# Performance work log

Measured on AMD Instinct MI355X. Metric: run time of the kernel, lower is better.

Reference implementation:

```python
import jax, jax.numpy as jnp
import numpy as np

B, T, C = 2, 2048, 1024
N_HEAD = 16
G_NON = 32   # qgroup_size_non (layernorm / residual path)
G_LIN = 32   # qgroup_size_lin (linear path)
QMAX = 127.0
EPS = 1e-5


def quantize(x, G):
    """Group-wise symmetric int8 quantization along the last dim.
    Returns q (int8, same shape as x) and scales s with shape x.shape[:-1] + (D//G,)."""
    shp = x.shape
    xg = x.reshape(shp[:-1] + (shp[-1] // G, G))
    s = jnp.maximum(jnp.max(jnp.abs(xg), axis=-1) / QMAX, 1e-8)
    q = jnp.clip(jnp.round(xg / s[..., None]), -QMAX, QMAX).astype(jnp.int8)
    return q.reshape(shp), s


def dequant(q, s, G):
    shp = q.shape
    xg = q.astype(jnp.float32).reshape(shp[:-1] + (shp[-1] // G, G)) * s[..., None]
    return xg.reshape(shp)


def quant_dequant(x, G):
    """Fake-quantize (straight-through): forward = dequant(quantize(x))."""
    q, s = quantize(x, G)
    xd = dequant(q, s, G)
    return x + jax.lax.stop_gradient(xd - x)


def setup_inputs() -> dict:
    key = jax.random.key(0)
    k1, k2, k3, k4 = jax.random.split(key, 4)
    x = jax.random.normal(k1, (B, T, C), dtype=jnp.float32)
    # LN stats of x, produced by the previous block's int8_add_..._MeanVar
    mean = jnp.mean(x, axis=-1)
    rstd = 1.0 / jnp.sqrt(jnp.var(x, axis=-1) + EPS)
    qx, sx = quantize(x, G_NON)
    ln_w = 1.0 + 0.02 * jax.random.normal(k2, (C,), dtype=jnp.float32)
    w1 = 0.02 * jax.random.normal(k3, (3 * C, C), dtype=jnp.float32)   # c_attn.weight [out,in]
    w2 = 0.02 * jax.random.normal(k4, (C, C), dtype=jnp.float32)       # c_proj.weight [out,in]
    return {"x": x, "qx": qx.astype(jnp.int32), "sx": sx, "mean": mean,
            "rstd": rstd, "ln_w": ln_w, "w1": w1, "w2": w2}


def reference(x, qx, sx, mean, rstd, ln_w, w1, w2):
    hd = C // N_HEAD
    # ---- Part1: int8 layernorm (uses provided mean/rstd) + int8 c_attn linear ----
    ln_in = dequant(qx.astype(jnp.int8), sx, G_NON)               # [B,T,C]
    h = (ln_in - mean[..., None]) * rstd[..., None] * ln_w        # layernorm output
    hq = quant_dequant(h, G_NON)                                  # requantize activations
    w1q = quant_dequant(w1, G_LIN)                                # int8 weight
    qkv = jnp.einsum('btc,oc->bto', hq, w1q)                      # [B,T,3C]
    q, k, v = jnp.split(qkv, 3, axis=-1)
    q = q.reshape(B, T, N_HEAD, hd).transpose(0, 2, 1, 3)         # [B,H,T,hd]
    k = k.reshape(B, T, N_HEAD, hd).transpose(0, 2, 1, 3)
    v = v.reshape(B, T, N_HEAD, hd).transpose(0, 2, 1, 3)
    # ---- causal SDPA ----
    scores = jnp.einsum('bhqd,bhkd->bhqk', q, k) / jnp.sqrt(jnp.float32(hd))
    causal = jnp.tril(jnp.ones((T, T), dtype=bool))
    scores = jnp.where(causal, scores, jnp.float32(-1e30))
    attn = jax.nn.softmax(scores, axis=-1)
    y = jnp.einsum('bhqk,bhkd->bhqd', attn, v)
    y = y.transpose(0, 2, 1, 3).reshape(B, T, C)
    # ---- Part2: int8 c_proj linear + residual add with mean/var ----
    yq = quant_dequant(y, G_LIN)
    w2q = quant_dequant(w2, G_LIN)
    proj = jnp.einsum('btc,oc->bto', yq, w2q)
    fpx = x + proj                                                # fp residual output
    mean_o = jnp.mean(fpx, axis=-1)
    rstd_o = 1.0 / jnp.sqrt(jnp.var(fpx, axis=-1) + EPS)
    qo, so = quantize(fpx, G_NON)                                 # quantized output for next block
    return (fpx, qo, so, mean_o, rstd_o)
```

## Files before the change

kernel.cpp:

```cpp
#include <hip/hip_runtime.h>
#include <stdint.h>

#define BB 2
#define TT 2048
#define CC 1024
#define NH 16
#define HD 64
#define NG 32
#define ROWS (BB*TT)
#define C3 (3*CC)

typedef _Float16 half_t;
typedef __attribute__((ext_vector_type(8))) _Float16 half8;
typedef __attribute__((ext_vector_type(2))) __fp16 fp16x2;
typedef __attribute__((ext_vector_type(4))) float f32x4;

#define GLDS16(g, l) __builtin_amdgcn_global_load_lds( \
    (__attribute__((address_space(1))) void*)(g), \
    (__attribute__((address_space(3))) void*)(l), 16, 0, 0)

#define LOG2E 1.44269504f
#define DEFER_THR 5.5451774f

__device__ __forceinline__ uint32_t pk_h2(float a, float b) {
  union { fp16x2 h; uint32_t u; } cv;
  cv.h = __builtin_amdgcn_cvt_pkrtz(a, b);
  return cv.u;
}

__global__ void k_qdq_w(const float* __restrict__ w1, const float* __restrict__ w2,
                        half_t* __restrict__ o1, half_t* __restrict__ o2) {
  int g = blockIdx.x * blockDim.x + threadIdx.x;
  const float* src; half_t* dst; int gl;
  if (g < C3 * NG) { src = w1; dst = o1; gl = g; }
  else             { src = w2; dst = o2; gl = g - C3 * NG; }
  const float4* p = reinterpret_cast<const float4*>(src + (size_t)gl * 32);
  float v[32]; float amax = 0.f;
  #pragma unroll
  for (int i = 0; i < 8; ++i) {
    float4 t = p[i];
    v[4*i] = t.x; v[4*i+1] = t.y; v[4*i+2] = t.z; v[4*i+3] = t.w;
    amax = fmaxf(amax, fmaxf(fmaxf(fabsf(t.x), fabsf(t.y)), fmaxf(fabsf(t.z), fabsf(t.w))));
  }
  float s = fmaxf(amax / 127.0f, 1e-8f);
  half_t* o = dst + (size_t)gl * 32;
  #pragma unroll
  for (int c = 0; c < 4; ++c) {
    half8 ov;
    #pragma unroll
    for (int j = 0; j < 8; ++j) {
      float q = fminf(fmaxf(rintf(v[c*8+j] / s), -127.f), 127.f);
      ov[j] = (half_t)(q * s);
    }
    *reinterpret_cast<half8*>(o + c*8) = ov;
  }
}

__global__ void k_qh(const int* __restrict__ qx, const float* __restrict__ sx,
                     const float* __restrict__ mean, const float* __restrict__ rstd,
                     const float* __restrict__ lnw, half_t* __restrict__ h16) {
  int g = blockIdx.x * blockDim.x + threadIdx.x;
  if (g >= ROWS * NG) return;
  int row = g >> 5, grp = g & 31;
  float sxv = sx[g];
  float mu = mean[row], rs = rstd[row];
  const int4* qp = reinterpret_cast<const int4*>(qx + (size_t)row * CC + grp * 32);
  const float4* wp = reinterpret_cast<const float4*>(lnw + grp * 32);
  float v[32]; float amax = 0.f;
  #pragma unroll
  for (int i = 0; i < 8; ++i) {
    int4 qv = qp[i]; float4 wv = wp[i];
    float h0 = ((float)qv.x * sxv - mu) * rs * wv.x;
    float h1 = ((float)qv.y * sxv - mu) * rs * wv.y;
    float h2 = ((float)qv.z * sxv - mu) * rs * wv.z;
    float h3 = ((float)qv.w * sxv - mu) * rs * wv.w;
    v[4*i] = h0; v[4*i+1] = h1; v[4*i+2] = h2; v[4*i+3] = h3;
    amax = fmaxf(amax, fmaxf(fmaxf(fabsf(h0), fabsf(h1)), fmaxf(fabsf(h2), fabsf(h3))));
  }
  float s = fmaxf(amax / 127.0f, 1e-8f);
  half_t* o = h16 + (size_t)row * CC + grp * 32;
  #pragma unroll
  for (int c = 0; c < 4; ++c) {
    half8 ov;
    #pragma unroll
    for (int j = 0; j < 8; ++j) {
      float q = fminf(fmaxf(rintf(v[c*8+j] / s), -127.f), 127.f);
      ov[j] = (half_t)(q * s);
    }
    *reinterpret_cast<half8*>(o + c*8) = ov;
  }
}

template<typename TO>
__global__ __launch_bounds__(256) void k_gemm16(const half_t* __restrict__ A,
                                                const half_t* __restrict__ B,
                                                TO* __restrict__ Out, int N) {
  __shared__ __align__(16) half_t As[128*32];
  __shared__ __align__(16) half_t Bs[128*32];
  const int tid = threadIdx.x;
  const int wave = tid >> 6, lane = tid & 63;
  const int l15 = lane & 15, lg = lane >> 4;
  const int m0 = blockIdx.y * 128, n0 = blockIdx.x * 128;
  const int wm = (wave >> 1) * 64, wn = (wave & 1) * 64;
  f32x4 acc[4][4];
  #pragma unroll
  for (int i = 0; i < 4; ++i)
    #pragma unroll
    for (int j = 0; j < 4; ++j) acc[i][j] = f32x4{0.f, 0.f, 0.f, 0.f};
  const int srow = lane >> 2;
  const int scol = (lane & 3) * 8;
  const int seg0 = wave * 2;
  for (int k0 = 0; k0 < 1024; k0 += 32) {
    #pragma unroll
    for (int s = 0; s < 2; ++s) {
      const int seg = seg0 + s;
      GLDS16(A + (size_t)(m0 + seg*16 + srow) * 1024 + k0 + scol, As + seg*512);
      GLDS16(B + (size_t)(n0 + seg*16 + srow) * 1024 + k0 + scol, Bs + seg*512);
    }
    __syncthreads();
    half8 af[4], bf[4];
    #pragma unroll
    for (int i = 0; i < 4; ++i) {
      af[i] = *reinterpret_cast<const half8*>(As + (wm + i*16 + l15)*32 + lg*8);
      bf[i] = *reinterpret_cast<const half8*>(Bs + (wn + i*16 + l15)*32 + lg*8);
    }
    #pragma unroll
    for (int mi = 0; mi < 4; ++mi)
      #pragma unroll
      for (int ni = 0; ni < 4; ++ni)
        acc[mi][ni] = __builtin_amdgcn_mfma_f32_16x16x32_f16(af[mi], bf[ni], acc[mi][ni], 0, 0, 0);
    __syncthreads();
  }
  const int crow = m0 + wm + lg * 4;
  const int ccol = n0 + wn + l15;
  #pragma unroll
  for (int mi = 0; mi < 4; ++mi)
    #pragma unroll
    for (int ni = 0; ni < 4; ++ni)
      #pragma unroll
      for (int r = 0; r < 4; ++r)
        Out[(size_t)(crow + mi*16 + r) * N + ccol + ni*16] = (TO)acc[mi][ni][r];
}

__global__ __launch_bounds__(256) void k_attn16(const half_t* __restrict__ qkv,
                                                half_t* __restrict__ y16) {
  __shared__ __align__(16) half_t Ks[64*72];
  __shared__ __align__(16) half_t Vt[64*72];
  __shared__ __align__(16) half_t Ps[4][16*72];
  const int tid = threadIdx.x;
  const int wave = tid >> 6, lane = tid & 63;
  const int l15 = lane & 15, lg = lane >> 4;
  const int bh = blockIdx.x, b = bh >> 4, h = bh & 15;
  const int j = blockIdx.y;
  const int qtA = j, qtB = 31 - j;

  const size_t rowA = (size_t)(b * TT + qtA * 64 + wave * 16 + l15);
  const size_t rowB = (size_t)(b * TT + qtB * 64 + wave * 16 + l15);
  const half_t* qpA = qkv + rowA * C3 + h * HD + lg * 8;
  const half_t* qpB = qkv + rowB * C3 + h * HD + lg * 8;
  const half8 qa0 = *reinterpret_cast<const half8*>(qpA)      * (half_t)0.125f;
  const half8 qa1 = *reinterpret_cast<const half8*>(qpA + 32) * (half_t)0.125f;
  const half8 qb0 = *reinterpret_cast<const half8*>(qpB)      * (half_t)0.125f;
  const half8 qb1 = *reinterpret_cast<const half8*>(qpB + 32) * (half_t)0.125f;

  float mA = -3.0e38f, lA = 0.f, mB = -3.0e38f, lB = 0.f;
  f32x4 ya[4], yb[4];
  #pragma unroll
  for (int n = 0; n < 4; ++n) { ya[n] = f32x4{0,0,0,0}; yb[n] = f32x4{0,0,0,0}; }

  const int sj = tid >> 2, sc = (tid & 3) * 16;
  const int vk = (tid >> 3) * 2, vd0 = (tid & 7) * 8;
  const int vxor = ((vd0 >> 3) & 7) << 2;
  half_t* pw = &Ps[wave][0];
  uint32_t* vt32 = reinterpret_cast<uint32_t*>(Vt);

  auto do_tile = [&](const half8& q0, const half8& q1, int kt, int qt,
                     float& m, float& l, f32x4* yacc) {
    f32x4 sacc[4];
    #pragma unroll
    for (int kg = 0; kg < 4; ++kg) sacc[kg] = f32x4{0,0,0,0};
    #pragma unroll
    for (int kg = 0; kg < 4; ++kg) {
      const half8 a0 = *reinterpret_cast<const half8*>(Ks + (kg*16 + l15)*72 + lg*8);
      const half8 a1 = *reinterpret_cast<const half8*>(Ks + (kg*16 + l15)*72 + lg*8 + 32);
      sacc[kg] = __builtin_amdgcn_mfma_f32_16x16x32_f16(a0, q0, sacc[kg], 0, 0, 0);
      sacc[kg] = __builtin_amdgcn_mfma_f32_16x16x32_f16(a1, q1, sacc[kg], 0, 0, 0);
    }
    float sv[16]; float tm = -3.0e38f;
    const bool diag = (kt == qt);
    #pragma unroll
    for (int kg = 0; kg < 4; ++kg)
      #pragma unroll
      for (int r = 0; r < 4; ++r) {
        float s = sacc[kg][r];
        if (diag && (kg*16 + lg*4 + r > wave*16 + l15)) s = -1e30f;
        sv[kg*4 + r] = s;
        tm = fmaxf(tm, s);
      }
    tm = fmaxf(tm, __shfl_xor(tm, 16));
    tm = fmaxf(tm, __shfl_xor(tm, 32));
    if (!__all(tm <= m + DEFER_THR)) {
      const float mn = fmaxf(m, tm);
      const float alpha = exp2f((m - mn) * LOG2E);
      l *= alpha;
      #pragma unroll
      for (int n = 0; n < 4; ++n) yacc[n] *= alpha;
      m = mn;
    }
    const float nm = -m * LOG2E;
    float rs = 0.f;
    #pragma unroll
    for (int i = 0; i < 16; ++i) { sv[i] = exp2f(fmaf(sv[i], LOG2E, nm)); rs += sv[i]; }
    rs += __shfl_xor(rs, 16);
    rs += __shfl_xor(rs, 32);
    l += rs;
    uint32_t* pd = reinterpret_cast<uint32_t*>(pw) + l15*36 + lg*2;
    #pragma unroll
    for (int kg = 0; kg < 4; ++kg) {
      pd[kg*8 + 0] = pk_h2(sv[kg*4 + 0], sv[kg*4 + 1]);
      pd[kg*8 + 1] = pk_h2(sv[kg*4 + 2], sv[kg*4 + 3]);
    }
    asm volatile("" ::: "memory");
    const half8 pb0 = *reinterpret_cast<const half8*>(pw + l15*72 + lg*8);
    const half8 pb1 = *reinterpret_cast<const half8*>(pw + l15*72 + lg*8 + 32);
    #pragma unroll
    for (int n = 0; n < 4; ++n) {
      const int d = n*16 + l15;
      const int x = ((n*2 + (l15 >> 3)) & 7) << 2;
      const int dw0 = (d*36 + lg*4) ^ x;
      const int dw1 = (d*36 + 16 + lg*4) ^ x;
      const half8 va0 = *reinterpret_cast<const half8*>(vt32 + dw0);
      const half8 va1 = *reinterpret_cast<const half8*>(vt32 + dw1);
      yacc[n] = __builtin_amdgcn_mfma_f32_16x16x32_f16(va0, pb0, yacc[n], 0, 0, 0);
      yacc[n] = __builtin_amdgcn_mfma_f32_16x16x32_f16(va1, pb1, yacc[n], 0, 0, 0);
    }
  };

  const half_t* kvb = qkv + ((size_t)b * TT) * C3 + CC + h * HD;
  for (int kt = 0; kt <= qtB; ++kt) {
    const half_t* kp = kvb + (size_t)(kt*64 + sj) * C3 + sc;
    const half8 k0 = *reinterpret_cast<const half8*>(kp);
    const half8 k1 = *reinterpret_cast<const half8*>(kp + 8);
    const half_t* vp = kvb + (size_t)(kt*64 + vk) * C3 + CC + vd0;
    const half8 v0 = *reinterpret_cast<const half8*>(vp);
    const half8 v1 = *reinterpret_cast<const half8*>(vp + C3);
    __syncthreads();
    *reinterpret_cast<half8*>(Ks + sj*72 + sc) = k0;
    *reinterpret_cast<half8*>(Ks + sj*72 + sc + 8) = k1;
    #pragma unroll
    for (int i = 0; i < 8; ++i) {
      const int d = vd0 + i;
      vt32[(d*36 + (vk >> 1)) ^ vxor] = pk_h2((float)v0[i], (float)v1[i]);
    }
    __syncthreads();
    do_tile(qb0, qb1, kt, qtB, mB, lB, yb);
    if (kt <= qtA) do_tile(qa0, qa1, kt, qtA, mA, lA, ya);
  }

  auto epi = [&](size_t row, float l, f32x4* yacc) {
    const float inv = 1.0f / l;
    float v[16];
    #pragma unroll
    for (int n = 0; n < 4; ++n)
      #pragma unroll
      for (int r = 0; r < 4; ++r) v[n*4 + r] = yacc[n][r] * inv;
    half_t* yp = y16 + row * CC + h * HD;
    #pragma unroll
    for (int g = 0; g < 2; ++g) {
      float am = 0.f;
      #pragma unroll
      for (int t = 0; t < 8; ++t) am = fmaxf(am, fabsf(v[g*8 + t]));
      am = fmaxf(am, __shfl_xor(am, 16));
      am = fmaxf(am, __shfl_xor(am, 32));
      const float s = fmaxf(am / 127.0f, 1e-8f);
      const float qi = 1.0f / s;
      #pragma unroll
      for (int nn = 0; nn < 2; ++nn) {
        const int n = g*2 + nn;
        union { half_t h4[4]; uint64_t u; } pk;
        #pragma unroll
        for (int r = 0; r < 4; ++r) {
          float q = fminf(fmaxf(rintf(v[n*4 + r] * qi), -127.f), 127.f);
          pk.h4[r] = (half_t)(q * s);
        }
        *reinterpret_cast<uint64_t*>(yp + n*16 + lg*4) = pk.u;
      }
    }
  };
  epi(rowB, lB, yb);
  epi(rowA, lA, ya);
}

__global__ __launch_bounds__(256) void k_final(
    const float* __restrict__ x, const half_t* __restrict__ proj,
    float* __restrict__ out_fpx, float* __restrict__ out_qo, float* __restrict__ out_so,
    float* __restrict__ out_mean, float* __restrict__ out_rstd) {
  __shared__ float red[16];
  int row = blockIdx.x;
  int tid = threadIdx.x;
  size_t base = (size_t)row * CC + tid * 4;
  float4 xv = *reinterpret_cast<const float4*>(x + base);
  union { uint64_t u; half_t h[4]; } pp;
  pp.u = *reinterpret_cast<const uint64_t*>(proj + base);
  float4 f;
  f.x = xv.x + (float)pp.h[0]; f.y = xv.y + (float)pp.h[1];
  f.z = xv.z + (float)pp.h[2]; f.w = xv.w + (float)pp.h[3];
  *reinterpret_cast<float4*>(out_fpx + base) = f;
  float sum = f.x + f.y + f.z + f.w;
  float sq  = f.x*f.x + f.y*f.y + f.z*f.z + f.w*f.w;
  #pragma unroll
  for (int off = 1; off < 64; off <<= 1) {
    sum += __shfl_xor(sum, off);
    sq  += __shfl_xor(sq, off);
  }
  int wid = tid >> 6, lane = tid & 63;
  if (lane == 0) { red[wid] = sum; red[8 + wid] = sq; }
  __syncthreads();
  if (tid == 0) {
    float s4 = red[0] + red[1] + red[2] + red[3];
    float q4 = red[8] + red[9] + red[10] + red[11];
    float mu = s4 * (1.0f / CC);
    float var = q4 * (1.0f / CC) - mu * mu;
    out_mean[row] = mu;
    out_rstd[row] = 1.0f / sqrtf(var + 1e-5f);
  }
  float amax = fmaxf(fmaxf(fabsf(f.x), fabsf(f.y)), fmaxf(fabsf(f.z), fabsf(f.w)));
  #pragma unroll
  for (int off = 1; off < 8; off <<= 1) amax = fmaxf(amax, __shfl_xor(amax, off, 8));
  float s = fmaxf(amax / 127.0f, 1e-8f);
  int g = tid >> 3, li = tid & 7;
  if (li == 0) out_so[row * NG + g] = s;
  float4 qo;
  qo.x = fminf(fmaxf(rintf(f.x / s), -127.f), 127.f);
  qo.y = fminf(fmaxf(rintf(f.y / s), -127.f), 127.f);
  qo.z = fminf(fmaxf(rintf(f.z / s), -127.f), 127.f);
  qo.w = fminf(fmaxf(rintf(f.w / s), -127.f), 127.f);
  *reinterpret_cast<float4*>(out_qo + base) = qo;
}

extern "C" void kernel_launch(void* const* d_in, const int* in_sizes, int n_in,
                              void* d_out, int out_size, void* d_ws, size_t ws_size,
                              hipStream_t stream) {
  const float* x    = (const float*)d_in[0];
  const int*   qx   = (const int*)d_in[1];
  const float* sx   = (const float*)d_in[2];
  const float* mean = (const float*)d_in[3];
  const float* rstd = (const float*)d_in[4];
  const float* lnw  = (const float*)d_in[5];
  const float* w1   = (const float*)d_in[6];
  const float* w2   = (const float*)d_in[7];

  float* out = (float*)d_out;
  float* o_fpx  = out;
  float* o_qo   = o_fpx + (size_t)ROWS * CC;
  float* o_so   = o_qo  + (size_t)ROWS * CC;
  float* o_mean = o_so  + (size_t)ROWS * NG;
  float* o_rstd = o_mean + ROWS;

  size_t off = 0;
  char* wsb = (char*)d_ws;
  auto alloc = [&](size_t bytes) -> void* {
    void* p = wsb + off;
    off += (bytes + 255) & ~(size_t)255;
    return p;
  };
  half_t* h16   = (half_t*)alloc((size_t)ROWS * CC * 2);
  half_t* w116  = (half_t*)alloc((size_t)C3 * CC * 2);
  half_t* w216  = (half_t*)alloc((size_t)CC * CC * 2);
  half_t* qkv16 = (half_t*)alloc((size_t)ROWS * C3 * 2);
  half_t* y16   = (half_t*)alloc((size_t)ROWS * CC * 2);
  half_t* proj  = (half_t*)alloc((size_t)ROWS * CC * 2);

  k_qdq_w<<<(C3 * NG + CC * NG) / 256, 256, 0, stream>>>(w1, w2, w116, w216);
  k_qh<<<(ROWS * NG) / 256, 256, 0, stream>>>(qx, sx, mean, rstd, lnw, h16);
  k_gemm16<half_t><<<dim3(C3 / 128, ROWS / 128), 256, 0, stream>>>(h16, w116, qkv16, C3);
  k_attn16<<<dim3(BB * NH, 16), 256, 0, stream>>>(qkv16, y16);
  k_gemm16<half_t><<<dim3(CC / 128, ROWS / 128), 256, 0, stream>>>(y16, w216, proj, CC);
  k_final<<<ROWS, 256, 0, stream>>>(x, proj, o_fpx, o_qo, o_so, o_mean, o_rstd);
}
```

Before: 142.5 us.

## Prefetch next K/V tile, interleave two query tiles, compute row sums via MFMA

The attention kernel now loads the next K/V tile into registers while the current tile is being computed, so global latency is hidden behind MFMA work. It also issues both query tiles' QK^T before either softmax, and gives each its own P buffer so the two streams can overlap. The softmax row sum is now accumulated with an extra MFMA against a vector of ones instead of shuffle reductions. Other changes: exp2 via the hardware builtin, V transpose via byte permutes instead of float conversions, precomputed V LDS offsets, and s_setprio around MFMA blocks. The cost is more registers and LDS, which may reduce occupancy, and the row sums are now taken from fp16-rounded P values.

```diff
diff --git a/kernel.cpp b/kernel.cpp
--- a/kernel.cpp
+++ b/kernel.cpp
@@ -48,9 +48,9 @@
   for (int c = 0; c < 4; ++c) {
     half8 ov;
     #pragma unroll
-    for (int j = 0; j < 8; ++j) {
-      float q = fminf(fmaxf(rintf(v[c*8+j] / s), -127.f), 127.f);
-      ov[j] = (half_t)(q * s);
+    for (int jj = 0; jj < 8; ++jj) {
+      float q = fminf(fmaxf(rintf(v[c*8+jj] / s), -127.f), 127.f);
+      ov[jj] = (half_t)(q * s);
     }
     *reinterpret_cast<half8*>(o + c*8) = ov;
   }
@@ -83,9 +83,9 @@
   for (int c = 0; c < 4; ++c) {
     half8 ov;
     #pragma unroll
-    for (int j = 0; j < 8; ++j) {
-      float q = fminf(fmaxf(rintf(v[c*8+j] / s), -127.f), 127.f);
-      ov[j] = (half_t)(q * s);
+    for (int jj = 0; jj < 8; ++jj) {
+      float q = fminf(fmaxf(rintf(v[c*8+jj] / s), -127.f), 127.f);
+      ov[jj] = (half_t)(q * s);
     }
     *reinterpret_cast<half8*>(o + c*8) = ov;
   }
@@ -106,7 +106,7 @@
   #pragma unroll
   for (int i = 0; i < 4; ++i)
     #pragma unroll
-    for (int j = 0; j < 4; ++j) acc[i][j] = f32x4{0.f, 0.f, 0.f, 0.f};
+    for (int jj = 0; jj < 4; ++jj) acc[i][jj] = f32x4{0.f, 0.f, 0.f, 0.f};
   const int srow = lane >> 2;
   const int scol = (lane & 3) * 8;
   const int seg0 = wave * 2;
@@ -146,7 +146,8 @@
                                                 half_t* __restrict__ y16) {
   __shared__ __align__(16) half_t Ks[64*72];
   __shared__ __align__(16) half_t Vt[64*72];
-  __shared__ __align__(16) half_t Ps[4][16*72];
+  __shared__ __align__(16) half_t PsA[4][16*72];
+  __shared__ __align__(16) half_t PsB[4][16*72];
   const int tid = threadIdx.x;
   const int wave = tid >> 6, lane = tid & 63;
   const int l15 = lane & 15, lg = lane >> 4;
@@ -163,31 +164,61 @@
   const half8 qb0 = *reinterpret_cast<const half8*>(qpB)      * (half_t)0.125f;
   const half8 qb1 = *reinterpret_cast<const half8*>(qpB + 32) * (half_t)0.125f;
 
-  float mA = -3.0e38f, lA = 0.f, mB = -3.0e38f, lB = 0.f;
+  float mA = -3.0e38f, mB = -3.0e38f;
   f32x4 ya[4], yb[4];
+  f32x4 laA = f32x4{0,0,0,0}, laB = f32x4{0,0,0,0};
   #pragma unroll
   for (int n = 0; n < 4; ++n) { ya[n] = f32x4{0,0,0,0}; yb[n] = f32x4{0,0,0,0}; }
 
   const int sj = tid >> 2, sc = (tid & 3) * 16;
   const int vk = (tid >> 3) * 2, vd0 = (tid & 7) * 8;
   const int vxor = ((vd0 >> 3) & 7) << 2;
-  half_t* pw = &Ps[wave][0];
+  const int kp2 = vk >> 1;
+  half_t* pwA = &PsA[wave][0];
+  half_t* pwB = &PsB[wave][0];
   uint32_t* vt32 = reinterpret_cast<uint32_t*>(Vt);
 
-  auto do_tile = [&](const half8& q0, const half8& q1, int kt, int qt,
-                     float& m, float& l, f32x4* yacc) {
-    f32x4 sacc[4];
-    #pragma unroll
-    for (int kg = 0; kg < 4; ++kg) sacc[kg] = f32x4{0,0,0,0};
+  int vdw0[4], vdw1[4];
+  #pragma unroll
+  for (int n = 0; n < 4; ++n) {
+    const int d = n*16 + l15;
+    const int x = ((n*2 + (l15 >> 3)) & 7) << 2;
+    vdw0[n] = (d*36 + lg*4) ^ x;
+    vdw1[n] = (d*36 + 16 + lg*4) ^ x;
+  }
+
+  half8 ones8;
+  #pragma unroll
+  for (int i = 0; i < 8; ++i) ones8[i] = (half_t)1.0f;
+
+  half8 k0r, k1r; uint4 u0r, u1r;
+  const half_t* kvb = qkv + ((size_t)b * TT) * C3 + CC + h * HD;
+  auto kload = [&](int kt) {
+    const half_t* kp = kvb + (size_t)(kt*64 + sj) * C3 + sc;
+    k0r = *reinterpret_cast<const half8*>(kp);
+    k1r = *reinterpret_cast<const half8*>(kp + 8);
+    const half_t* vp = kvb + (size_t)(kt*64 + vk) * C3 + CC + vd0;
+    u0r = *reinterpret_cast<const uint4*>(vp);
+    u1r = *reinterpret_cast<const uint4*>(vp + C3);
+  };
+
+  auto qkt = [&](f32x4* sacc, const half8 q0, const half8 q1) {
+    __builtin_amdgcn_s_setprio(1);
     #pragma unroll
     for (int kg = 0; kg < 4; ++kg) {
       const half8 a0 = *reinterpret_cast<const half8*>(Ks + (kg*16 + l15)*72 + lg*8);
       const half8 a1 = *reinterpret_cast<const half8*>(Ks + (kg*16 + l15)*72 + lg*8 + 32);
-      sacc[kg] = __builtin_amdgcn_mfma_f32_16x16x32_f16(a0, q0, sacc[kg], 0, 0, 0);
-      sacc[kg] = __builtin_amdgcn_mfma_f32_16x16x32_f16(a1, q1, sacc[kg], 0, 0, 0);
-    }
+      f32x4 t = f32x4{0,0,0,0};
+      t = __builtin_amdgcn_mfma_f32_16x16x32_f16(a0, q0, t, 0, 0, 0);
+      t = __builtin_amdgcn_mfma_f32_16x16x32_f16(a1, q1, t, 0, 0, 0);
+      sacc[kg] = t;
+    }
+    __builtin_amdgcn_s_setprio(0);
+  };
+
+  auto finish = [&](f32x4* sacc, bool diag, half_t* pw,
+                    float& m, f32x4& lacc, f32x4* yacc) {
     float sv[16]; float tm = -3.0e38f;
-    const bool diag = (kt == qt);
     #pragma unroll
     for (int kg = 0; kg < 4; ++kg)
       #pragma unroll
@@ -201,60 +232,61 @@
     tm = fmaxf(tm, __shfl_xor(tm, 32));
     if (!__all(tm <= m + DEFER_THR)) {
       const float mn = fmaxf(m, tm);
-      const float alpha = exp2f((m - mn) * LOG2E);
-      l *= alpha;
+      const float alpha = __builtin_amdgcn_exp2f((m - mn) * LOG2E);
       #pragma unroll
       for (int n = 0; n < 4; ++n) yacc[n] *= alpha;
+      lacc *= alpha;
       m = mn;
     }
     const float nm = -m * LOG2E;
-    float rs = 0.f;
-    #pragma unroll
-    for (int i = 0; i < 16; ++i) { sv[i] = exp2f(fmaf(sv[i], LOG2E, nm)); rs += sv[i]; }
-    rs += __shfl_xor(rs, 16);
-    rs += __shfl_xor(rs, 32);
-    l += rs;
+    #pragma unroll
+    for (int i = 0; i < 16; ++i)
+      sv[i] = __builtin_amdgcn_exp2f(fmaf(sv[i], LOG2E, nm));
     uint32_t* pd = reinterpret_cast<uint32_t*>(pw) + l15*36 + lg*2;
     #pragma unroll
     for (int kg = 0; kg < 4; ++kg) {
       pd[kg*8 + 0] = pk_h2(sv[kg*4 + 0], sv[kg*4 + 1]);
       pd[kg*8 + 1] = pk_h2(sv[kg*4 + 2], sv[kg*4 + 3]);
     }
-    asm volatile("" ::: "memory");
+    __builtin_amdgcn_sched_barrier(0);
     const half8 pb0 = *reinterpret_cast<const half8*>(pw + l15*72 + lg*8);
     const half8 pb1 = *reinterpret_cast<const half8*>(pw + l15*72 + lg*8 + 32);
+    __builtin_amdgcn_s_setprio(1);
     #pragma unroll
     for (int n = 0; n < 4; ++n) {
-      const int d = n*16 + l15;
-      const int x = ((n*2 + (l15 >> 3)) & 7) << 2;
-      const int dw0 = (d*36 + lg*4) ^ x;
-      const int dw1 = (d*36 + 16 + lg*4) ^ x;
-      const half8 va0 = *reinterpret_cast<const half8*>(vt32 + dw0);
-      const half8 va1 = *reinterpret_cast<const half8*>(vt32 + dw1);
+      const half8 va0 = *reinterpret_cast<const half8*>(vt32 + vdw0[n]);
+      const half8 va1 = *reinterpret_cast<const half8*>(vt32 + vdw1[n]);
       yacc[n] = __builtin_amdgcn_mfma_f32_16x16x32_f16(va0, pb0, yacc[n], 0, 0, 0);
       yacc[n] = __builtin_amdgcn_mfma_f32_16x16x32_f16(va1, pb1, yacc[n], 0, 0, 0);
     }
+    lacc = __builtin_amdgcn_mfma_f32_16x16x32_f16(ones8, pb0, lacc, 0, 0, 0);
+    lacc = __builtin_amdgcn_mfma_f32_16x16x32_f16(ones8, pb1, lacc, 0, 0, 0);
+    __builtin_amdgcn_s_setprio(0);
   };
 
-  const half_t* kvb = qkv + ((size_t)b * TT) * C3 + CC + h * HD;
+  kload(0);
   for (int kt = 0; kt <= qtB; ++kt) {
-    const half_t* kp = kvb + (size_t)(kt*64 + sj) * C3 + sc;
-    const half8 k0 = *reinterpret_cast<const half8*>(kp);
-    const half8 k1 = *reinterpret_cast<const half8*>(kp + 8);
-    const half_t* vp = kvb + (size_t)(kt*64 + vk) * C3 + CC + vd0;
-    const half8 v0 = *reinterpret_cast<const half8*>(vp);
-    const half8 v1 = *reinterpret_cast<const half8*>(vp + C3);
     __syncthreads();
-    *reinterpret_cast<half8*>(Ks + sj*72 + sc) = k0;
-    *reinterpret_cast<half8*>(Ks + sj*72 + sc + 8) = k1;
-    #pragma unroll
-    for (int i = 0; i < 8; ++i) {
-      const int d = vd0 + i;
-      vt32[(d*36 + (vk >> 1)) ^ vxor] = pk_h2((float)v0[i], (float)v1[i]);
+    *reinterpret_cast<half8*>(Ks + sj*72 + sc) = k0r;
+    *reinterpret_cast<half8*>(Ks + sj*72 + sc + 8) = k1r;
+    {
+      const uint32_t w0[4] = {u0r.x, u0r.y, u0r.z, u0r.w};
+      const uint32_t w1[4] = {u1r.x, u1r.y, u1r.z, u1r.w};
+      #pragma unroll
+      for (int i = 0; i < 4; ++i) {
+        const int d = vd0 + 2*i;
+        vt32[(d*36 + kp2) ^ vxor]       = __builtin_amdgcn_perm(w1[i], w0[i], 0x05040100u);
+        vt32[((d+1)*36 + kp2) ^ vxor]   = __builtin_amdgcn_perm(w1[i], w0[i], 0x07060302u);
+      }
     }
     __syncthreads();
-    do_tile(qb0, qb1, kt, qtB, mB, lB, yb);
-    if (kt <= qtA) do_tile(qa0, qa1, kt, qtA, mA, lA, ya);
+    if (kt < qtB) kload(kt + 1);
+    const bool actA = (kt <= qtA);
+    f32x4 sB[4], sA[4];
+    qkt(sB, qb0, qb1);
+    if (actA) qkt(sA, qa0, qa1);
+    finish(sB, kt == qtB, pwB, mB, laB, yb);
+    if (actA) finish(sA, kt == qtA, pwA, mA, laA, ya);
   }
 
   auto epi = [&](size_t row, float l, f32x4* yacc) {
@@ -287,8 +319,8 @@
       }
     }
   };
-  epi(rowB, lB, yb);
-  epi(rowA, lA, ya);
+  epi(rowB, laB[0], yb);
+  epi(rowA, laA[0], ya);
 }
 
 __global__ __launch_bounds__(256) void k_final(
```

Result: faster. 132.7 us (-6.9%).
